# Performance work log

Measured on AMD Instinct MI355X. Metric: run time of the kernel, lower is better.

Reference implementation:

```python
import jax, jax.numpy as jnp
import numpy as np

B, T_ENC, T_DEC = 16, 256, 200
N_MELS, ENC_DIM, PRENET, ARNN, DRNN, ATT, NF, KS = 80, 512, 256, 1024, 1024, 128, 32, 31


def _init(k, shape, fan_in):
    return jax.random.normal(k, shape, dtype=jnp.float32) / np.sqrt(fan_in).astype(np.float32)


def setup_inputs() -> dict:
    ks = jax.random.split(jax.random.key(0), 20)
    return {
        "memory": jax.random.normal(ks[0], (B, T_ENC, ENC_DIM), jnp.float32),
        "decoder_inputs": jax.random.normal(ks[1], (B, N_MELS, T_DEC), jnp.float32),
        "memory_lengths": jax.random.randint(ks[2], (B,), T_ENC // 2, T_ENC + 1),
        "prenet_W1": _init(ks[3], (N_MELS, PRENET), N_MELS),
        "prenet_W2": _init(ks[4], (PRENET, PRENET), PRENET),
        "arnn_Wih": _init(ks[5], (PRENET + ENC_DIM, 4 * ARNN), PRENET + ENC_DIM),
        "arnn_Whh": _init(ks[6], (ARNN, 4 * ARNN), ARNN),
        "arnn_b": jnp.zeros((4 * ARNN,), jnp.float32),
        "Wq": _init(ks[7], (ARNN, ATT), ARNN),
        "Wmem": _init(ks[8], (ENC_DIM, ATT), ENC_DIM),
        "v_w": _init(ks[9], (ATT,), ATT),
        "loc_conv_W": _init(ks[10], (NF, 2, KS), 2 * KS),
        "loc_dense_W": _init(ks[11], (NF, ATT), NF),
        "drnn_Wih": _init(ks[12], (ARNN + ENC_DIM, 4 * DRNN), ARNN + ENC_DIM),
        "drnn_Whh": _init(ks[13], (DRNN, 4 * DRNN), DRNN),
        "drnn_b": jnp.zeros((4 * DRNN,), jnp.float32),
        "proj_W": _init(ks[14], (DRNN + ENC_DIM, N_MELS), DRNN + ENC_DIM),
        "proj_b": jnp.zeros((N_MELS,), jnp.float32),
        "gate_W": _init(ks[15], (DRNN + ENC_DIM, 1), DRNN + ENC_DIM),
        "gate_b": jnp.zeros((1,), jnp.float32),
    }


def _lstm_cell(x, h, c, Wih, Whh, b):
    z = x @ Wih + h @ Whh + b  # [B, 4H], torch gate order i,f,g,o
    i, f, g, o = jnp.split(z, 4, axis=-1)
    c_new = jax.nn.sigmoid(f) * c + jax.nn.sigmoid(i) * jnp.tanh(g)
    h_new = jax.nn.sigmoid(o) * jnp.tanh(c_new)
    return h_new, c_new


def reference(memory, decoder_inputs, memory_lengths, prenet_W1, prenet_W2,
              arnn_Wih, arnn_Whh, arnn_b, Wq, Wmem, v_w, loc_conv_W, loc_dense_W,
              drnn_Wih, drnn_Whh, drnn_b, proj_W, proj_b, gate_W, gate_b):
    dt = memory.dtype
    # parse_decoder_inputs + go-frame: [T_DEC+1, B, n_mels]
    di = jnp.transpose(decoder_inputs, (2, 0, 1))
    di = jnp.concatenate([jnp.zeros((1, B, N_MELS), dt), di], axis=0)
    # prenet (dropout hardcoded training=True in source; deterministic key here)
    k1, k2 = jax.random.split(jax.random.key(42))
    x = jax.nn.relu(di @ prenet_W1)
    x = x * jax.random.bernoulli(k1, 0.5, x.shape).astype(dt) * 2.0
    x = jax.nn.relu(x @ prenet_W2)
    x = x * jax.random.bernoulli(k2, 0.5, x.shape).astype(dt) * 2.0
    pre = x[:-1]  # [T_DEC, B, PRENET] (loop consumes first T_DEC frames)

    pm = memory @ Wmem  # processed_memory [B, T_enc, ATT]
    pad_mask = jnp.arange(T_ENC)[None, :] >= memory_lengths[:, None]  # [B, T_enc]
    pad = KS // 2

    def step(carry, xt):
        ah, ac, dh, dc, aw, awc, ctx = carry
        ah, ac = _lstm_cell(jnp.concatenate([xt, ctx], -1), ah, ac, arnn_Wih, arnn_Whh, arnn_b)
        # location-sensitive attention
        awcat = jnp.stack([aw, awc], axis=1)  # [B, 2, T_enc]
        loc = jax.lax.conv_general_dilated(awcat, loc_conv_W, (1,), [(pad, pad)],
                                           dimension_numbers=("NCH", "OIH", "NCH"))  # [B, NF, T_enc]
        loc = jnp.swapaxes(loc, 1, 2) @ loc_dense_W  # [B, T_enc, ATT]
        pq = ah @ Wq  # [B, ATT]
        e = jnp.tanh(pq[:, None, :] + loc + pm) @ v_w  # [B, T_enc]
        e = jnp.where(pad_mask, jnp.asarray(-1e9, dt), e)
        w = jax.nn.softmax(e, axis=1)
        ctx = jnp.einsum("bt,bte->be", w, memory)
        awc = awc + w
        dh, dc = _lstm_cell(jnp.concatenate([ah, ctx], -1), dh, dc, drnn_Wih, drnn_Whh, drnn_b)
        dhc = jnp.concatenate([dh, ctx], axis=1)
        mel = dhc @ proj_W + proj_b  # [B, n_mels]
        gate = (dhc @ gate_W + gate_b)[:, 0]  # [B]
        return (ah, ac, dh, dc, w, awc, ctx), (mel, gate, w)

    carry0 = (jnp.zeros((B, ARNN), dt), jnp.zeros((B, ARNN), dt),
              jnp.zeros((B, DRNN), dt), jnp.zeros((B, DRNN), dt),
              jnp.zeros((B, T_ENC), dt), jnp.zeros((B, T_ENC), dt),
              jnp.zeros((B, ENC_DIM), dt))
    _, (mels, gates, aligns) = jax.lax.scan(step, carry0, pre)
    mel_out = jnp.transpose(mels, (1, 2, 0))    # [B, n_mels, T_DEC]
    gate_out = jnp.transpose(gates, (1, 0))     # [B, T_DEC]
    align_out = jnp.transpose(aligns, (1, 0, 2))  # [B, T_DEC, T_enc]
    return mel_out, gate_out, align_out
```

## Files before the change

kernel.cpp:

```cpp
#include <hip/hip_runtime.h>
#include <stdint.h>

typedef unsigned short u16;
typedef _Float16 h2f16 __attribute__((ext_vector_type(2)));

#define BB    16
#define TENC  256
#define TDEC  200
#define NMELS 80
#define EDIM  512
#define PREN  256
#define ARN   1024
#define ATTN  128
#define NFILT 32
#define KSIZE 31

#define NBLK  256
#define NTHR  1024

#define OFF_AW     0
#define OFF_AWC    4096
#define OFF_AC     8192
#define OFF_DC     24576
#define OFF_XCAT1  49152
#define OFF_XCAT2  77824
#define STATE_F    118784
#define OFF_PRETU  118784
#define OFF_PMU    528384
#define OFF_Z      790528
#define OFF_PQP    1314816
#define OFF_EBUF   1347584
#define OFF_BAR    1351680

__host__ __device__ inline void tf2x32(uint32_t k0, uint32_t k1, uint32_t x0, uint32_t x1,
                                       uint32_t &y0, uint32_t &y1) {
  uint32_t ks2 = k0 ^ k1 ^ 0x1BD11BDAu;
  x0 += k0; x1 += k1;
  const int R0[4] = {13, 15, 26, 6};
  const int R1[4] = {17, 29, 16, 24};
#pragma unroll
  for (int g = 0; g < 5; ++g) {
    const int *R = (g & 1) ? R1 : R0;
#pragma unroll
    for (int i = 0; i < 4; ++i) {
      x0 += x1;
      x1 = (x1 << R[i]) | (x1 >> (32 - R[i]));
      x1 ^= x0;
    }
    switch (g) {
      case 0: x0 += k1;  x1 += ks2 + 1u; break;
      case 1: x0 += ks2; x1 += k0 + 2u;  break;
      case 2: x0 += k0;  x1 += k1 + 3u;  break;
      case 3: x0 += k1;  x1 += ks2 + 4u; break;
      case 4: x0 += ks2; x1 += k0 + 5u;  break;
    }
  }
  y0 = x0; y1 = x1;
}

__device__ inline bool keep_mask(uint32_t k0, uint32_t k1, uint32_t idx) {
  uint32_t y0, y1;
  tf2x32(k0, k1, 0u, idx, y0, y1);
  return (((y0 ^ y1) >> 31) == 0u);
}

__device__ inline float bf2f(u16 v) {
  union { uint32_t u; float f; } x;
  x.u = ((uint32_t)v) << 16;
  return x.f;
}
__device__ inline u16 f2bf(float f) {
  union { float f; uint32_t u; } x;
  x.f = f;
  uint32_t r = ((x.u >> 16) & 1u) + 0x7FFFu;
  return (u16)((x.u + r) >> 16);
}
__device__ inline float sigm(float x) { return 1.f / (1.f + __expf(-x)); }
__device__ inline float ftanh(float x) {
  x = fminf(fmaxf(x, -15.f), 15.f);
  float e = __expf(2.f * x);
  return (e - 1.f) / (e + 1.f);
}

__device__ inline uint32_t packh2(float a, float b) {
  h2f16 h; h[0] = (_Float16)a; h[1] = (_Float16)b;
  union { h2f16 h; uint32_t u; } x; x.h = h; return x.u;
}
__device__ inline h2f16 u2h2(uint32_t u) {
  union { uint32_t u; h2f16 h; } x; x.u = u; return x.h;
}
__device__ inline float fdot2(h2f16 a, h2f16 b, float c) {
#if __has_builtin(__builtin_amdgcn_fdot2)
  return __builtin_amdgcn_fdot2(a, b, c, false);
#else
  return (float)a[0] * (float)b[0] + (float)a[1] * (float)b[1] + c;
#endif
}

__device__ inline float cload(const float *p) {
  uint32_t u = __hip_atomic_load((uint32_t *)p, __ATOMIC_RELAXED,
                                 __HIP_MEMORY_SCOPE_SYSTEM);
  union { uint32_t u; float f; } x; x.u = u; return x.f;
}
__device__ inline void cstore(float *p, float v) {
  union { float f; uint32_t u; } x; x.f = v;
  __hip_atomic_store((uint32_t *)p, x.u, __ATOMIC_RELAXED,
                     __HIP_MEMORY_SCOPE_SYSTEM);
}

__device__ inline void gsync(unsigned int *bar, unsigned int e, int cb) {
  __syncthreads();
  if (threadIdx.x == 0) {
    asm volatile("s_waitcnt vmcnt(0)" ::: "memory");
    int g = cb & 7;
    unsigned int *arr = bar + g * 64;
    unsigned int *gct = bar + 512;
    unsigned int *rel = bar + 576 + g * 64;
    unsigned int old = __hip_atomic_fetch_add(arr, 1u, __ATOMIC_RELAXED,
                                              __HIP_MEMORY_SCOPE_SYSTEM);
    if (old == e * 32u - 1u) {
      unsigned int o2 = __hip_atomic_fetch_add(gct, 1u, __ATOMIC_RELAXED,
                                               __HIP_MEMORY_SCOPE_SYSTEM);
      if (o2 == e * 8u - 1u) {
#pragma unroll
        for (int g2 = 0; g2 < 8; ++g2)
          __hip_atomic_store(bar + 576 + g2 * 64, e, __ATOMIC_RELAXED,
                             __HIP_MEMORY_SCOPE_SYSTEM);
      }
    }
    while (__hip_atomic_load(rel, __ATOMIC_RELAXED, __HIP_MEMORY_SCOPE_SYSTEM) < e)
      __builtin_amdgcn_s_sleep(1);
  }
  __syncthreads();
}

__global__ __launch_bounds__(256) void k_prenet1(const float *__restrict__ dec_in,
                                                 const float *__restrict__ W1,
                                                 u16 *__restrict__ x1,
                                                 uint32_t k0, uint32_t k1) {
  int bid = blockIdx.x;
  int t = bid >> 4, b = bid & 15;
  int tid = threadIdx.x;
  __shared__ float di[NMELS];
  if (tid < NMELS)
    di[tid] = (t == 0) ? 0.f : dec_in[((size_t)b * NMELS + tid) * TDEC + (t - 1)];
  __syncthreads();
  int j = tid;
  float acc = 0.f;
#pragma unroll 4
  for (int m = 0; m < NMELS; ++m) acc += di[m] * W1[(size_t)m * PREN + j];
  acc = fmaxf(acc, 0.f);
  uint32_t idx = ((uint32_t)(t * BB + b)) * PREN + (uint32_t)j;
  acc = keep_mask(k0, k1, idx) ? acc * 2.f : 0.f;
  x1[(t * BB + b) * PREN + j] = f2bf(acc);
}

__global__ __launch_bounds__(256) void k_prenet2(const u16 *__restrict__ x1,
                                                 const float *__restrict__ W2,
                                                 u16 *__restrict__ preTu,
                                                 float *__restrict__ xpre0,
                                                 uint32_t k0, uint32_t k1) {
  int bid = blockIdx.x;
  int t = bid >> 4, b = bid & 15;
  int tid = threadIdx.x;
  __shared__ float xl[PREN];
  xl[tid] = bf2f(x1[(t * BB + b) * PREN + tid]);
  __syncthreads();
  int j = tid;
  float acc = 0.f;
#pragma unroll 4
  for (int k = 0; k < PREN; ++k) acc += xl[k] * W2[(size_t)k * PREN + j];
  acc = fmaxf(acc, 0.f);
  uint32_t idx = ((uint32_t)(t * BB + b)) * PREN + (uint32_t)j;
  acc = keep_mask(k0, k1, idx) ? acc * 2.f : 0.f;
  preTu[(size_t)t * 4096 + j * 16 + b] = f2bf(acc);
  if (t == 0) xpre0[j * 16 + b] = acc;
}

__global__ __launch_bounds__(256) void k_pm(const float *__restrict__ memory,
                                            const float *__restrict__ Wmem,
                                            u16 *__restrict__ pmu) {
  int p = blockIdx.x;
  int b = p & 15, jt = p >> 4;
  int tt = threadIdx.x;
  float acc[32];
#pragma unroll
  for (int j = 0; j < 32; ++j) acc[j] = 0.f;
  const float *mrow = memory + ((size_t)b * TENC + tt) * EDIM;
  const float *wb = Wmem + jt * 32;
  for (int e = 0; e < EDIM; ++e) {
    float mv = mrow[e];
    const float *wr = wb + (size_t)e * ATTN;
#pragma unroll
    for (int j = 0; j < 32; ++j) acc[j] += mv * wr[j];
  }
#pragma unroll
  for (int j = 0; j < 32; ++j)
    pmu[((size_t)(b * ATTN + jt * 32 + j)) * TENC + tt] = f2bf(acc[j]);
}

struct F2 { float x, y; };

union Scr {
  uint32_t xs1[112 * 16];
  uint32_t xs2[160 * 16];
  struct { F2 part[16 * 64]; float hn[64]; } al;
  struct {
    float aw_l[96], awc_l[96];
    float lc[64 * 33];
    float pq[128];
    float ep[64 * 17];
  } att;
  struct { float e_l[256]; float red[32]; float smax, sinv; float part[32 * 33]; } ctc;
  struct { float xl[1536]; float part[12 * 81]; } out;
};

struct KArgs {
  const float *memory; const int *mlen;
  const float *aWih, *aWhh, *ab;
  const float *Wq, *vw, *convW, *ldW;
  const float *dWih, *dWhh, *db;
  const float *projW, *projB, *gateW, *gateB;
  const u16 *preTu, *pmu;
  float *aw, *awc, *ac, *dc, *xcat1, *xcat2, *z, *pqp, *ebuf;
  unsigned int *bar;
  float *mel, *gate, *algn;
};

__global__ __launch_bounds__(NTHR) void k_persist(KArgs A) {
  __shared__ uint32_t w1h[112 * 128];
  __shared__ uint32_t w2h[160 * 128];
  __shared__ Scr s;
  const int cb = blockIdx.x;
  const int tid = threadIdx.x;
  const int q = cb >> 5;
  const int c = cb & 31;

  for (int i = tid; i < 112 * 128; i += NTHR) {
    int k2 = i >> 7, col = i & 127, cg = c * 128 + col;
    int r0 = q * 224 + k2 * 2;
    float f0 = (r0 < 768) ? A.aWih[(size_t)r0 * 4096 + cg]
                          : A.aWhh[(size_t)(r0 - 768) * 4096 + cg];
    float f1 = (r0 + 1 < 768) ? A.aWih[(size_t)(r0 + 1) * 4096 + cg]
                              : A.aWhh[(size_t)(r0 - 767) * 4096 + cg];
    w1h[i] = packh2(f0, f1);
  }
  for (int i = tid; i < 160 * 128; i += NTHR) {
    int k2 = i >> 7, col = i & 127, cg = c * 128 + col;
    int r0 = q * 320 + k2 * 2;
    float f0 = (r0 < 1536) ? A.dWih[(size_t)r0 * 4096 + cg]
                           : A.dWhh[(size_t)(r0 - 1536) * 4096 + cg];
    float f1 = (r0 + 1 < 1536) ? A.dWih[(size_t)(r0 + 1) * 4096 + cg]
                               : A.dWhh[(size_t)(r0 - 1535) * 4096 + cg];
    w2h[i] = packh2(f0, f1);
  }
  __syncthreads();

  unsigned int ep = 0;
  for (int t = 0; t < TDEC; ++t) {
    for (int i = tid; i < 112 * 16; i += NTHR) {
      int k2 = i >> 4, b = i & 15;
      const float *xr = A.xcat1 + (size_t)(q * 224 + k2 * 2) * 16 + b;
      s.xs1[i] = packh2(cload(xr), cload(xr + 16));
    }
    __syncthreads();
    {
      int col = tid & 127, bg = tid >> 7;
      float a0 = 0.f, a1 = 0.f;
      const uint32_t *wp = w1h + col;
      const uint32_t *xp = s.xs1 + bg * 2;
#pragma unroll 8
      for (int k2 = 0; k2 < 112; ++k2) {
        h2f16 w = u2h2(wp[k2 * 128]);
        a0 = fdot2(w, u2h2(xp[k2 * 16]), a0);
        a1 = fdot2(w, u2h2(xp[k2 * 16 + 1]), a1);
      }
      int cg = c * 128 + col;
      cstore(&A.z[((size_t)q * 16 + bg * 2    ) * 4096 + cg], a0);
      cstore(&A.z[((size_t)q * 16 + bg * 2 + 1) * 4096 + cg], a1);
    }
    gsync(A.bar, ++ep, cb);

    {
      int b = cb & 15, ug = cb >> 4;
      {
        int u_l = tid & 63, j = tid >> 6;
        int kc = j & 7, gh = j >> 3;
        const float *zb = A.z + ((size_t)(kc * 16 + b)) * 4096 + gh * 2048 + (ug * 64 + u_l);
        F2 p; p.x = cload(zb); p.y = cload(zb + 1024);
        s.al.part[j * 64 + u_l] = p;
      }
      __syncthreads();
      if (tid < 64) {
        int uu = ug * 64 + tid;
        float g0 = 0.f, g1 = 0.f, g2 = 0.f, g3 = 0.f;
#pragma unroll
        for (int kc = 0; kc < 8; ++kc) {
          F2 v0 = s.al.part[kc * 64 + tid];
          F2 v1 = s.al.part[(8 + kc) * 64 + tid];
          g0 += v0.x; g1 += v0.y; g2 += v1.x; g3 += v1.y;
        }
        float zi = g0 + A.ab[uu], zf = g1 + A.ab[1024 + uu];
        float zg = g2 + A.ab[2048 + uu], zo = g3 + A.ab[3072 + uu];
        float cn = sigm(zf) * A.ac[b * 1024 + uu] + sigm(zi) * ftanh(zg);
        float hn = sigm(zo) * ftanh(cn);
        A.ac[b * 1024 + uu] = cn;
        cstore(&A.xcat1[(size_t)(768 + uu) * 16 + b], hn);
        cstore(&A.xcat2[(size_t)uu * 16 + b], hn);
        s.al.hn[tid] = hn;
      }
      __syncthreads();
      if (tid < 128) {
        float a = 0.f;
        const float *wq = A.Wq + (size_t)(ug * 64) * 128 + tid;
#pragma unroll 4
        for (int k = 0; k < 64; ++k) a += s.al.hn[k] * wq[(size_t)k * 128];
        cstore(&A.pqp[(size_t)(b * 16 + ug) * 128 + tid], a);
      }
    }
    gsync(A.bar, ++ep, cb);

    if (cb < 64) {
      int b = cb & 15, tq = cb >> 4;
      if (tid < 96) {
        int gi = tq * 64 - 16 + tid;
        bool ok = (gi >= 0 && gi < 256);
        s.att.aw_l[tid]  = ok ? cload(&A.aw[b * 256 + gi])  : 0.f;
        s.att.awc_l[tid] = ok ? cload(&A.awc[b * 256 + gi]) : 0.f;
      }
      if (tid >= 128 && tid < 256) {
        int j = tid - 128;
        float sum = 0.f;
#pragma unroll
        for (int g = 0; g < 16; ++g) sum += cload(&A.pqp[(size_t)(b * 16 + g) * 128 + j]);
        s.att.pq[j] = sum;
      }
      __syncthreads();
      {
        int tt_l = tid & 63, fg = tid >> 6;
        int f0 = fg * 2;
        float a0 = 0.f, a1 = 0.f;
        for (int k = 0; k < KSIZE; ++k) {
          float av = s.att.aw_l[tt_l + k + 1];
          float cv = s.att.awc_l[tt_l + k + 1];
          a0 += av * A.convW[f0 * 62 + k]       + cv * A.convW[f0 * 62 + 31 + k];
          a1 += av * A.convW[(f0 + 1) * 62 + k] + cv * A.convW[(f0 + 1) * 62 + 31 + k];
        }
        s.att.lc[tt_l * 33 + f0]     = a0;
        s.att.lc[tt_l * 33 + f0 + 1] = a1;
      }
      __syncthreads();
      {
        int tt_l = tid & 63, g = tid >> 6;
        int tt = tq * 64 + tt_l, j0 = g * 8;
        float acc[8] = {0, 0, 0, 0, 0, 0, 0, 0};
        for (int f = 0; f < NFILT; ++f) {
          float lv = s.att.lc[tt_l * 33 + f];
          const float *lw = A.ldW + f * ATTN + j0;
#pragma unroll
          for (int jj = 0; jj < 8; ++jj) acc[jj] += lv * lw[jj];
        }
        float es = 0.f;
#pragma unroll
        for (int jj = 0; jj < 8; ++jj) {
          float sv = acc[jj] + s.att.pq[j0 + jj]
                   + bf2f(A.pmu[((size_t)(b * 128 + j0 + jj)) * 256 + tt]);
          es += ftanh(sv) * A.vw[j0 + jj];
        }
        s.att.ep[tt_l * 17 + g] = es;
      }
      __syncthreads();
      if (tid < 64) {
        float e = 0.f;
#pragma unroll
        for (int g = 0; g < 16; ++g) e += s.att.ep[tid * 17 + g];
        int tt = tq * 64 + tid;
        if (tt >= A.mlen[b]) e = -1e9f;
        cstore(&A.ebuf[b * 256 + tt], e);
      }
    }
    gsync(A.bar, ++ep, cb);

    {
      int b = cb & 15, ec = cb >> 4;
      if (tid < 256) s.ctc.e_l[tid] = cload(&A.ebuf[b * 256 + tid]);
      __syncthreads();
      if (tid < 32) {
        float m = -1e30f;
#pragma unroll
        for (int i = 0; i < 8; ++i) m = fmaxf(m, s.ctc.e_l[tid * 8 + i]);
        s.ctc.red[tid] = m;
      }
      __syncthreads();
      if (tid == 0) {
        float m = -1e30f;
        for (int i = 0; i < 32; ++i) m = fmaxf(m, s.ctc.red[i]);
        s.ctc.smax = m;
      }
      __syncthreads();
      if (tid < 256) s.ctc.e_l[tid] = __expf(s.ctc.e_l[tid] - s.ctc.smax);
      __syncthreads();
      if (tid < 32) {
        float sm = 0.f;
#pragma unroll
        for (int i = 0; i < 8; ++i) sm += s.ctc.e_l[tid * 8 + i];
        s.ctc.red[tid] = sm;
      }
      __syncthreads();
      if (tid == 0) {
        float sm = 0.f;
        for (int i = 0; i < 32; ++i) sm += s.ctc.red[i];
        s.ctc.sinv = 1.f / sm;
      }
      __syncthreads();
      if (tid < 256) s.ctc.e_l[tid] *= s.ctc.sinv;
      __syncthreads();
      if (ec == 0 && tid < 256) {
        float w = s.ctc.e_l[tid];
        cstore(&A.aw[b * 256 + tid], w);
        cstore(&A.awc[b * 256 + tid], cload(&A.awc[b * 256 + tid]) + w);
        A.algn[((size_t)b * TDEC + t) * TENC + tid] = w;
      }
      {
        int e_l = tid & 31, sub = tid >> 5;
        const float *mp = A.memory + ((size_t)(b * 256) + sub * 8) * 512 + ec * 32 + e_l;
        float a = 0.f;
#pragma unroll
        for (int i = 0; i < 8; ++i) a += s.ctc.e_l[sub * 8 + i] * mp[(size_t)i * 512];
        s.ctc.part[e_l * 33 + sub] = a;
      }
      __syncthreads();
      if (tid < 32) {
        float sum = 0.f;
#pragma unroll
        for (int i = 0; i < 32; ++i) sum += s.ctc.part[tid * 33 + i];
        int eg = ec * 32 + tid;
        cstore(&A.xcat1[(size_t)(256 + eg) * 16 + b], sum);
        cstore(&A.xcat2[(size_t)(1024 + eg) * 16 + b], sum);
      }
    }
    gsync(A.bar, ++ep, cb);

    for (int i = tid; i < 160 * 16; i += NTHR) {
      int k2 = i >> 4, b = i & 15;
      const float *xr = A.xcat2 + (size_t)(q * 320 + k2 * 2) * 16 + b;
      s.xs2[i] = packh2(cload(xr), cload(xr + 16));
    }
    __syncthreads();
    {
      int col = tid & 127, bg = tid >> 7;
      float a0 = 0.f, a1 = 0.f;
      const uint32_t *wp = w2h + col;
      const uint32_t *xp = s.xs2 + bg * 2;
#pragma unroll 8
      for (int k2 = 0; k2 < 160; ++k2) {
        h2f16 w = u2h2(wp[k2 * 128]);
        a0 = fdot2(w, u2h2(xp[k2 * 16]), a0);
        a1 = fdot2(w, u2h2(xp[k2 * 16 + 1]), a1);
      }
      int cg = c * 128 + col;
      cstore(&A.z[((size_t)q * 16 + bg * 2    ) * 4096 + cg], a0);
      cstore(&A.z[((size_t)q * 16 + bg * 2 + 1) * 4096 + cg], a1);
    }
    gsync(A.bar, ++ep, cb);

    if (cb < 16) {
      int b = cb;
      {
        int u = tid;
        float zi = 0.f, zf = 0.f, zg = 0.f, zo = 0.f;
        for (int kc = 0; kc < 8; ++kc) {
          const float *zb = A.z + ((size_t)(kc * 16 + b)) * 4096;
          zi += cload(zb + u); zf += cload(zb + u + 1024);
          zg += cload(zb + u + 2048); zo += cload(zb + u + 3072);
        }
        zi += A.db[u]; zf += A.db[u + 1024]; zg += A.db[u + 2048]; zo += A.db[u + 3072];
        float cn = sigm(zf) * A.dc[b * 1024 + u] + sigm(zi) * ftanh(zg);
        float hn = sigm(zo) * ftanh(cn);
        A.dc[b * 1024 + u] = cn;
        cstore(&A.xcat2[(size_t)(1536 + u) * 16 + b], hn);
        s.out.xl[u] = hn;
      }
      if (tid < 512) s.out.xl[1024 + tid] = cload(&A.xcat2[(size_t)(1024 + tid) * 16 + b]);
      __syncthreads();
      if (tid < 960) {
        int col = tid % 80, kc = tid / 80;
        const float *wp = A.projW + (size_t)(kc * 128) * 80 + col;
        const float *xk = s.out.xl + kc * 128;
        float a = 0.f;
#pragma unroll 4
        for (int kk = 0; kk < 128; ++kk) a += xk[kk] * wp[(size_t)kk * 80];
        s.out.part[kc * 81 + col] = a;
      } else if (tid < 972) {
        int kc = tid - 960;
        const float *xk = s.out.xl + kc * 128;
        const float *gk = A.gateW + kc * 128;
        float a = 0.f;
#pragma unroll 4
        for (int kk = 0; kk < 128; ++kk) a += xk[kk] * gk[kk];
        s.out.part[kc * 81 + 80] = a;
      }
      __syncthreads();
      if (tid < 81) {
        float sum = 0.f;
#pragma unroll
        for (int kc = 0; kc < 12; ++kc) sum += s.out.part[kc * 81 + tid];
        if (tid < 80) A.mel[((size_t)b * 80 + tid) * TDEC + t] = sum + A.projB[tid];
        else          A.gate[(size_t)b * TDEC + t] = sum + A.gateB[0];
      }
    } else if (cb < 20) {
      if (t + 1 < TDEC) {
        int idx = (cb - 16) * 1024 + tid;
        cstore(&A.xcat1[idx], bf2f(A.preTu[(size_t)(t + 1) * 4096 + idx]));
      }
    }
    gsync(A.bar, ++ep, cb);
  }
}

extern "C" void kernel_launch(void *const *d_in, const int *in_sizes, int n_in,
                              void *d_out, int out_size, void *d_ws, size_t ws_size,
                              hipStream_t stream) {
  (void)in_sizes; (void)n_in; (void)out_size; (void)ws_size;
  const float *memory = (const float *)d_in[0];
  const float *dec_in = (const float *)d_in[1];
  const int   *mlen   = (const int *)d_in[2];
  const float *pw1    = (const float *)d_in[3];
  const float *pw2    = (const float *)d_in[4];
  const float *aWih   = (const float *)d_in[5];
  const float *aWhh   = (const float *)d_in[6];
  const float *ab     = (const float *)d_in[7];
  const float *wq     = (const float *)d_in[8];
  const float *wmem   = (const float *)d_in[9];
  const float *vw     = (const float *)d_in[10];
  const float *convW  = (const float *)d_in[11];
  const float *ldW    = (const float *)d_in[12];
  const float *dWih   = (const float *)d_in[13];
  const float *dWhh   = (const float *)d_in[14];
  const float *db     = (const float *)d_in[15];
  const float *projW  = (const float *)d_in[16];
  const float *projB  = (const float *)d_in[17];
  const float *gateW  = (const float *)d_in[18];
  const float *gateB  = (const float *)d_in[19];

  float *out_mel  = (float *)d_out;
  float *out_gate = out_mel + (size_t)16 * 80 * 200;
  float *out_algn = out_gate + (size_t)16 * 200;

  float *ws = (float *)d_ws;
  float *aw    = ws + OFF_AW;
  float *awc   = ws + OFF_AWC;
  float *ac    = ws + OFF_AC;
  float *dc    = ws + OFF_DC;
  float *xcat1 = ws + OFF_XCAT1;
  float *xcat2 = ws + OFF_XCAT2;
  float *xpre  = xcat1;
  u16 *preTu = (u16 *)(ws + OFF_PRETU);
  u16 *pmu   = (u16 *)(ws + OFF_PMU);
  float *z    = ws + OFF_Z;
  float *pqp  = ws + OFF_PQP;
  float *ebuf = ws + OFF_EBUF;
  unsigned int *bar = (unsigned int *)(ws + OFF_BAR);
  u16 *x1u   = (u16 *)z;

  hipMemsetAsync(ws, 0, STATE_F * sizeof(float), stream);
  hipMemsetAsync(bar, 0, 2048 * sizeof(unsigned int), stream);

  uint32_t K1a, K1b, K2a, K2b;
  tf2x32(0u, 42u, 0u, 0u, K1a, K1b);
  tf2x32(0u, 42u, 0u, 1u, K2a, K2b);

  k_prenet1<<<TDEC * BB, 256, 0, stream>>>(dec_in, pw1, x1u, K1a, K1b);
  k_prenet2<<<TDEC * BB, 256, 0, stream>>>(x1u, pw2, preTu, xpre, K2a, K2b);
  k_pm<<<64, 256, 0, stream>>>(memory, wmem, pmu);

  KArgs ka;
  ka.memory = memory; ka.mlen = mlen;
  ka.aWih = aWih; ka.aWhh = aWhh; ka.ab = ab;
  ka.Wq = wq; ka.vw = vw; ka.convW = convW; ka.ldW = ldW;
  ka.dWih = dWih; ka.dWhh = dWhh; ka.db = db;
  ka.projW = projW; ka.projB = projB; ka.gateW = gateW; ka.gateB = gateB;
  ka.preTu = preTu; ka.pmu = pmu;
  ka.aw = aw; ka.awc = awc; ka.ac = ac; ka.dc = dc;
  ka.xcat1 = xcat1; ka.xcat2 = xcat2; ka.z = z; ka.pqp = pqp; ka.ebuf = ebuf;
  ka.bar = bar;
  ka.mel = out_mel; ka.gate = out_gate; ka.algn = out_algn;

  void *kp[] = { &ka };
  hipLaunchCooperativeKernel((void *)k_persist, dim3(NBLK), dim3(NTHR), kp, 0, stream);
}
```

Baseline: 27.28 ms.

## Restructure persistent decoder to unit-sliced LSTM columns with fewer grid barriers

```diff
diff --git a/kernel.cpp b/kernel.cpp
--- a/kernel.cpp
+++ b/kernel.cpp
@@ -18,19 +18,16 @@
 #define NBLK  256
 #define NTHR  1024
 
-#define OFF_AW     0
-#define OFF_AWC    4096
-#define OFF_AC     8192
-#define OFF_DC     24576
-#define OFF_XCAT1  49152
-#define OFF_XCAT2  77824
-#define STATE_F    118784
-#define OFF_PRETU  118784
-#define OFF_PMU    528384
-#define OFF_Z      790528
-#define OFF_PQP    1314816
-#define OFF_EBUF   1347584
-#define OFF_BAR    1351680
+#define OFF_X1H   0
+#define OFF_X2H   22528
+#define OFF_AHF   51200
+#define OFF_CTXF  67584
+#define OFF_DHF   83968
+#define OFF_BAR   100352
+#define STATE_F   102400
+#define OFF_PRETU 102400
+#define OFF_PMU   512000
+#define OFF_X1U   774144
 
 __host__ __device__ inline void tf2x32(uint32_t k0, uint32_t k1, uint32_t x0, uint32_t x1,
                                        uint32_t &y0, uint32_t &y1) {
@@ -98,14 +95,20 @@
 }
 
 __device__ inline float cload(const float *p) {
-  uint32_t u = __hip_atomic_load((uint32_t *)p, __ATOMIC_RELAXED,
-                                 __HIP_MEMORY_SCOPE_SYSTEM);
+  uint32_t u = __hip_atomic_load((const uint32_t *)p, __ATOMIC_RELAXED,
+                                 __HIP_MEMORY_SCOPE_AGENT);
   union { uint32_t u; float f; } x; x.u = u; return x.f;
 }
 __device__ inline void cstore(float *p, float v) {
   union { float f; uint32_t u; } x; x.f = v;
   __hip_atomic_store((uint32_t *)p, x.u, __ATOMIC_RELAXED,
-                     __HIP_MEMORY_SCOPE_SYSTEM);
+                     __HIP_MEMORY_SCOPE_AGENT);
+}
+__device__ inline uint32_t cload_u32(const uint32_t *p) {
+  return __hip_atomic_load(p, __ATOMIC_RELAXED, __HIP_MEMORY_SCOPE_AGENT);
+}
+__device__ inline void cstore_u32(uint32_t *p, uint32_t v) {
+  __hip_atomic_store(p, v, __ATOMIC_RELAXED, __HIP_MEMORY_SCOPE_AGENT);
 }
 
 __device__ inline void gsync(unsigned int *bar, unsigned int e, int cb) {
@@ -117,18 +120,18 @@
     unsigned int *gct = bar + 512;
     unsigned int *rel = bar + 576 + g * 64;
     unsigned int old = __hip_atomic_fetch_add(arr, 1u, __ATOMIC_RELAXED,
-                                              __HIP_MEMORY_SCOPE_SYSTEM);
+                                              __HIP_MEMORY_SCOPE_AGENT);
     if (old == e * 32u - 1u) {
       unsigned int o2 = __hip_atomic_fetch_add(gct, 1u, __ATOMIC_RELAXED,
-                                               __HIP_MEMORY_SCOPE_SYSTEM);
+                                               __HIP_MEMORY_SCOPE_AGENT);
       if (o2 == e * 8u - 1u) {
 #pragma unroll
         for (int g2 = 0; g2 < 8; ++g2)
           __hip_atomic_store(bar + 576 + g2 * 64, e, __ATOMIC_RELAXED,
-                             __HIP_MEMORY_SCOPE_SYSTEM);
+                             __HIP_MEMORY_SCOPE_AGENT);
       }
     }
-    while (__hip_atomic_load(rel, __ATOMIC_RELAXED, __HIP_MEMORY_SCOPE_SYSTEM) < e)
+    while (__hip_atomic_load(rel, __ATOMIC_RELAXED, __HIP_MEMORY_SCOPE_AGENT) < e)
       __builtin_amdgcn_s_sleep(1);
   }
   __syncthreads();
@@ -157,8 +160,8 @@
 
 __global__ __launch_bounds__(256) void k_prenet2(const u16 *__restrict__ x1,
                                                  const float *__restrict__ W2,
-                                                 u16 *__restrict__ preTu,
-                                                 float *__restrict__ xpre0,
+                                                 uint32_t *__restrict__ preTuP,
+                                                 uint32_t *__restrict__ x1hPre,
                                                  uint32_t k0, uint32_t k1) {
   int bid = blockIdx.x;
   int t = bid >> 4, b = bid & 15;
@@ -173,8 +176,12 @@
   acc = fmaxf(acc, 0.f);
   uint32_t idx = ((uint32_t)(t * BB + b)) * PREN + (uint32_t)j;
   acc = keep_mask(k0, k1, idx) ? acc * 2.f : 0.f;
-  preTu[(size_t)t * 4096 + j * 16 + b] = f2bf(acc);
-  if (t == 0) xpre0[j * 16 + b] = acc;
+  float accN = __shfl_down(acc, 1);
+  if (!(j & 1)) {
+    uint32_t pk = packh2(acc, accN);
+    preTuP[(size_t)t * 2048 + (j >> 1) * 16 + b] = pk;
+    if (t == 0) x1hPre[(j >> 1) * 16 + b] = pk;
+  }
 }
 
 __global__ __launch_bounds__(256) void k_pm(const float *__restrict__ memory,
@@ -199,19 +206,16 @@
     pmu[((size_t)(b * ATTN + jt * 32 + j)) * TENC + tt] = f2bf(acc[j]);
 }
 
-struct F2 { float x, y; };
-
 union Scr {
-  uint32_t xs1[112 * 16];
-  uint32_t xs2[160 * 16];
-  struct { F2 part[16 * 64]; float hn[64]; } al;
+  struct { uint32_t xs[2][1088]; float zr[1024]; } z;
   struct {
-    float aw_l[96], awc_l[96];
-    float lc[64 * 33];
+    float ah[1024];
+    union { float pqp[1024]; float cp[2][512]; } u;
     float pq[128];
-    float ep[64 * 17];
-  } att;
-  struct { float e_l[256]; float red[32]; float smax, sinv; float part[32 * 33]; } ctc;
+    float e_l[256];
+    float red[32];
+    float smax, sinv;
+  } at;
   struct { float xl[1536]; float part[12 * 81]; } out;
 };
 
@@ -221,301 +225,318 @@
   const float *Wq, *vw, *convW, *ldW;
   const float *dWih, *dWhh, *db;
   const float *projW, *projB, *gateW, *gateB;
-  const u16 *preTu, *pmu;
-  float *aw, *awc, *ac, *dc, *xcat1, *xcat2, *z, *pqp, *ebuf;
+  const uint32_t *preTuP; const u16 *pmu;
+  uint32_t *x1h, *x2h;
+  float *ahf, *ctxf, *dhf;
   unsigned int *bar;
   float *mel, *gate, *algn;
 };
 
+__device__ inline void do_out(const KArgs &A, Scr &s, int b, int tm, int tid) {
+  s.out.xl[tid] = cload(A.dhf + (size_t)tid * 16 + b);
+  if (tid < 512) s.out.xl[1024 + tid] = cload(A.ctxf + (size_t)(tm & 1) * 8192 + tid * 16 + b);
+  __syncthreads();
+  if (tid < 960) {
+    int col = tid % 80, kc = tid / 80;
+    const float *wp = A.projW + (size_t)(kc * 128) * 80 + col;
+    const float *xk = s.out.xl + kc * 128;
+    float a = 0.f;
+#pragma unroll 4
+    for (int kk = 0; kk < 128; ++kk) a += xk[kk] * wp[(size_t)kk * 80];
+    s.out.part[kc * 81 + col] = a;
+  } else if (tid < 972) {
+    int kc = tid - 960;
+    const float *xk = s.out.xl + kc * 128;
+    const float *gk = A.gateW + kc * 128;
+    float a = 0.f;
+#pragma unroll 4
+    for (int kk = 0; kk < 128; ++kk) a += xk[kk] * gk[kk];
+    s.out.part[kc * 81 + 80] = a;
+  }
+  __syncthreads();
+  if (tid < 81) {
+    float sum = 0.f;
+#pragma unroll
+    for (int kc = 0; kc < 12; ++kc) sum += s.out.part[kc * 81 + tid];
+    if (tid < 80) A.mel[((size_t)b * 80 + tid) * TDEC + tm] = sum + A.projB[tid];
+    else          A.gate[(size_t)b * TDEC + tm] = sum + A.gateB[0];
+  }
+}
+
 __global__ __launch_bounds__(NTHR) void k_persist(KArgs A) {
-  __shared__ uint32_t w1h[112 * 128];
-  __shared__ uint32_t w2h[160 * 128];
+  __shared__ uint32_t w1h[16 * 900];
+  __shared__ uint32_t w2h[16 * 1284];
+  __shared__ float awA[288], awC[288];
   __shared__ Scr s;
   const int cb = blockIdx.x;
   const int tid = threadIdx.x;
-  const int q = cb >> 5;
-  const int c = cb & 31;
-
-  for (int i = tid; i < 112 * 128; i += NTHR) {
-    int k2 = i >> 7, col = i & 127, cg = c * 128 + col;
-    int r0 = q * 224 + k2 * 2;
-    float f0 = (r0 < 768) ? A.aWih[(size_t)r0 * 4096 + cg]
-                          : A.aWhh[(size_t)(r0 - 768) * 4096 + cg];
-    float f1 = (r0 + 1 < 768) ? A.aWih[(size_t)(r0 + 1) * 4096 + cg]
-                              : A.aWhh[(size_t)(r0 - 767) * 4096 + cg];
-    w1h[i] = packh2(f0, f1);
-  }
-  for (int i = tid; i < 160 * 128; i += NTHR) {
-    int k2 = i >> 7, col = i & 127, cg = c * 128 + col;
-    int r0 = q * 320 + k2 * 2;
-    float f0 = (r0 < 1536) ? A.dWih[(size_t)r0 * 4096 + cg]
-                           : A.dWhh[(size_t)(r0 - 1536) * 4096 + cg];
-    float f1 = (r0 + 1 < 1536) ? A.dWih[(size_t)(r0 + 1) * 4096 + cg]
-                               : A.dWhh[(size_t)(r0 - 1535) * 4096 + cg];
-    w2h[i] = packh2(f0, f1);
-  }
+
+  for (int i = tid; i < 16 * 896; i += NTHR) {
+    int k2 = i >> 4, cl = i & 15;
+    int gcol = cb * 4 + (cl & 3) + (cl >> 2) * 1024;
+    int r0 = k2 * 2;
+    float f0 = (r0 < 768) ? A.aWih[(size_t)r0 * 4096 + gcol]
+                          : A.aWhh[(size_t)(r0 - 768) * 4096 + gcol];
+    float f1 = (r0 + 1 < 768) ? A.aWih[(size_t)(r0 + 1) * 4096 + gcol]
+                              : A.aWhh[(size_t)(r0 - 767) * 4096 + gcol];
+    w1h[cl * 900 + k2] = packh2(f0, f1);
+  }
+  for (int i = tid; i < 16 * 1280; i += NTHR) {
+    int k2 = i >> 4, cl = i & 15;
+    int gcol = cb * 4 + (cl & 3) + (cl >> 2) * 1024;
+    int r0 = k2 * 2;
+    float f0 = (r0 < 1536) ? A.dWih[(size_t)r0 * 4096 + gcol]
+                           : A.dWhh[(size_t)(r0 - 1536) * 4096 + gcol];
+    float f1 = (r0 + 1 < 1536) ? A.dWih[(size_t)(r0 + 1) * 4096 + gcol]
+                               : A.dWhh[(size_t)(r0 - 1535) * 4096 + gcol];
+    w2h[cl * 1284 + k2] = packh2(f0, f1);
+  }
+  if (tid < 288) { awA[tid] = 0.f; awC[tid] = 0.f; }
   __syncthreads();
 
+  const int cl = tid & 15, bq = (tid >> 4) & 15, sl = tid >> 8;
+  const int k2s = tid >> 4, bs = tid & 15;
+  float acR = 0.f, dcR = 0.f;
   unsigned int ep = 0;
+
   for (int t = 0; t < TDEC; ++t) {
-    for (int i = tid; i < 112 * 16; i += NTHR) {
-      int k2 = i >> 4, b = i & 15;
-      const float *xr = A.xcat1 + (size_t)(q * 224 + k2 * 2) * 16 + b;
-      s.xs1[i] = packh2(cload(xr), cload(xr + 16));
-    }
-    __syncthreads();
+    const int p = t & 1, rp = p ^ 1;
+
     {
-      int col = tid & 127, bg = tid >> 7;
-      float a0 = 0.f, a1 = 0.f;
-      const uint32_t *wp = w1h + col;
-      const uint32_t *xp = s.xs1 + bg * 2;
-#pragma unroll 8
-      for (int k2 = 0; k2 < 112; ++k2) {
-        h2f16 w = u2h2(wp[k2 * 128]);
-        a0 = fdot2(w, u2h2(xp[k2 * 16]), a0);
-        a1 = fdot2(w, u2h2(xp[k2 * 16 + 1]), a1);
-      }
-      int cg = c * 128 + col;
-      cstore(&A.z[((size_t)q * 16 + bg * 2    ) * 4096 + cg], a0);
-      cstore(&A.z[((size_t)q * 16 + bg * 2 + 1) * 4096 + cg], a1);
+      uint32_t v[14];
+#pragma unroll
+      for (int c = 0; c < 14; ++c) {
+        int K2 = c * 64 + k2s;
+        int pp = K2 < 384 ? K2 : 384 + rp * 512 + (K2 - 384);
+        v[c] = cload_u32(A.x1h + (size_t)pp * 16 + bs);
+      }
+      float acc = 0.f;
+      const uint32_t *wcol = w1h + cl * 900;
+#pragma unroll
+      for (int c = 0; c < 14; ++c) {
+        s.z.xs[c & 1][bs * 68 + k2s] = v[c];
+        __syncthreads();
+        const uint32_t *xr = s.z.xs[c & 1] + bq * 68 + sl * 16;
+        const uint32_t *wr = wcol + c * 64 + sl * 16;
+#pragma unroll
+        for (int kk = 0; kk < 16; kk += 4) {
+          uint4 wv = *(const uint4 *)(wr + kk);
+          uint4 xv = *(const uint4 *)(xr + kk);
+          acc = fdot2(u2h2(wv.x), u2h2(xv.x), acc);
+          acc = fdot2(u2h2(wv.y), u2h2(xv.y), acc);
+          acc = fdot2(u2h2(wv.z), u2h2(xv.z), acc);
+          acc = fdot2(u2h2(wv.w), u2h2(xv.w), acc);
+        }
+      }
+      s.z.zr[sl * 256 + cl * 16 + bq] = acc;
+      __syncthreads();
+      if (tid < 64) {
+        int ul = tid >> 4, bb = tid & 15, u = cb * 4 + ul;
+        float zg4[4];
+#pragma unroll
+        for (int gate = 0; gate < 4; ++gate) {
+          int cc = gate * 4 + ul;
+          float zs = A.ab[(size_t)gate * 1024 + u];
+#pragma unroll
+          for (int slc = 0; slc < 4; ++slc) zs += s.z.zr[slc * 256 + cc * 16 + bb];
+          zg4[gate] = zs;
+        }
+        float cn = sigm(zg4[1]) * acR + sigm(zg4[0]) * ftanh(zg4[2]);
+        float hn = sigm(zg4[3]) * ftanh(cn);
+        acR = cn;
+        cstore(A.ahf + (size_t)u * 16 + bb, hn);
+        float hn2 = __shfl_down(hn, 16);
+        if (!(ul & 1)) {
+          uint32_t pk = packh2(hn, hn2);
+          cstore_u32(A.x1h + (size_t)(384 + p * 512 + (u >> 1)) * 16 + bb, pk);
+          cstore_u32(A.x2h + (size_t)(u >> 1) * 16 + bb, pk);
+        }
+      }
     }
     gsync(A.bar, ++ep, cb);
 
-    {
-      int b = cb & 15, ug = cb >> 4;
+    if (cb < 16) {
+      int b = cb;
+      int len = A.mlen[b];
+      s.at.ah[tid] = cload(A.ahf + (size_t)tid * 16 + b);
+      __syncthreads();
       {
-        int u_l = tid & 63, j = tid >> 6;
-        int kc = j & 7, gh = j >> 3;
-        const float *zb = A.z + ((size_t)(kc * 16 + b)) * 4096 + gh * 2048 + (ug * 64 + u_l);
-        F2 p; p.x = cload(zb); p.y = cload(zb + 1024);
-        s.al.part[j * 64 + u_l] = p;
-      }
-      __syncthreads();
-      if (tid < 64) {
-        int uu = ug * 64 + tid;
-        float g0 = 0.f, g1 = 0.f, g2 = 0.f, g3 = 0.f;
-#pragma unroll
-        for (int kc = 0; kc < 8; ++kc) {
-          F2 v0 = s.al.part[kc * 64 + tid];
-          F2 v1 = s.al.part[(8 + kc) * 64 + tid];
-          g0 += v0.x; g1 += v0.y; g2 += v1.x; g3 += v1.y;
-        }
-        float zi = g0 + A.ab[uu], zf = g1 + A.ab[1024 + uu];
-        float zg = g2 + A.ab[2048 + uu], zo = g3 + A.ab[3072 + uu];
-        float cn = sigm(zf) * A.ac[b * 1024 + uu] + sigm(zi) * ftanh(zg);
-        float hn = sigm(zo) * ftanh(cn);
-        A.ac[b * 1024 + uu] = cn;
-        cstore(&A.xcat1[(size_t)(768 + uu) * 16 + b], hn);
-        cstore(&A.xcat2[(size_t)uu * 16 + b], hn);
-        s.al.hn[tid] = hn;
+        int j = tid & 127, kc = tid >> 7;
+        float a = 0.f;
+        const float *wq = A.Wq + (size_t)(kc * 128) * ATTN + j;
+#pragma unroll 4
+        for (int k = 0; k < 128; ++k) a += s.at.ah[kc * 128 + k] * wq[(size_t)k * ATTN];
+        s.at.u.pqp[j * 8 + kc] = a;
       }
       __syncthreads();
       if (tid < 128) {
+        float sm = 0.f;
+#pragma unroll
+        for (int kc = 0; kc < 8; ++kc) sm += s.at.u.pqp[tid * 8 + kc];
+        s.at.pq[tid] = sm;
+      }
+      __syncthreads();
+      int tt = tid >> 2, g = tid & 3;
+      float lc[8];
+#pragma unroll
+      for (int f8 = 0; f8 < 8; ++f8) lc[f8] = 0.f;
+      for (int k = 0; k < KSIZE; ++k) {
+        float av = awA[tt + k + 1], cv = awC[tt + k + 1];
+#pragma unroll
+        for (int f8 = 0; f8 < 8; ++f8) {
+          int f = g * 8 + f8;
+          lc[f8] += av * A.convW[f * 62 + k] + cv * A.convW[f * 62 + 31 + k];
+        }
+      }
+      float es = 0.f;
+#pragma unroll
+      for (int half = 0; half < 2; ++half) {
+        float loc[16];
+#pragma unroll
+        for (int jj = 0; jj < 16; ++jj) loc[jj] = 0.f;
+#pragma unroll
+        for (int r = 0; r < 4; ++r) {
+          int fg = g ^ r;
+#pragma unroll
+          for (int f8 = 0; f8 < 8; ++f8) {
+            float lv = __shfl_xor(lc[f8], r);
+            const float4 *lw4 =
+                (const float4 *)(A.ldW + (size_t)(fg * 8 + f8) * ATTN + g * 32 + half * 16);
+            float4 w0 = lw4[0], w1v = lw4[1], w2v = lw4[2], w3v = lw4[3];
+            loc[0] += lv * w0.x;  loc[1] += lv * w0.y;  loc[2] += lv * w0.z;  loc[3] += lv * w0.w;
+            loc[4] += lv * w1v.x; loc[5] += lv * w1v.y; loc[6] += lv * w1v.z; loc[7] += lv * w1v.w;
+            loc[8] += lv * w2v.x; loc[9] += lv * w2v.y; loc[10]+= lv * w2v.z; loc[11]+= lv * w2v.w;
+            loc[12]+= lv * w3v.x; loc[13]+= lv * w3v.y; loc[14]+= lv * w3v.z; loc[15]+= lv * w3v.w;
+          }
+        }
+#pragma unroll
+        for (int jj = 0; jj < 16; ++jj) {
+          int j = g * 32 + half * 16 + jj;
+          float sv = loc[jj] + s.at.pq[j] + bf2f(A.pmu[((size_t)(b * 128 + j)) * 256 + tt]);
+          es += ftanh(sv) * A.vw[j];
+        }
+      }
+      es += __shfl_xor(es, 1);
+      es += __shfl_xor(es, 2);
+      if (g == 0) s.at.e_l[tt] = (tt >= len) ? -1e9f : es;
+      __syncthreads();
+      if (tid < 32) {
+        float m = -1e30f;
+#pragma unroll
+        for (int i = 0; i < 8; ++i) m = fmaxf(m, s.at.e_l[tid * 8 + i]);
+        s.at.red[tid] = m;
+      }
+      __syncthreads();
+      if (tid == 0) {
+        float m = -1e30f;
+        for (int i = 0; i < 32; ++i) m = fmaxf(m, s.at.red[i]);
+        s.at.smax = m;
+      }
+      __syncthreads();
+      if (tid < 256) s.at.e_l[tid] = __expf(s.at.e_l[tid] - s.at.smax);
+      __syncthreads();
+      if (tid < 32) {
+        float sm = 0.f;
+#pragma unroll
+        for (int i = 0; i < 8; ++i) sm += s.at.e_l[tid * 8 + i];
+        s.at.red[tid] = sm;
+      }
+      __syncthreads();
+      if (tid == 0) {
+        float sm = 0.f;
+        for (int i = 0; i < 32; ++i) sm += s.at.red[i];
+        s.at.sinv = 1.f / sm;
+      }
+      __syncthreads();
+      if (tid < 256) {
+        float w = s.at.e_l[tid] * s.at.sinv;
+        s.at.e_l[tid] = w;
+        awA[16 + tid] = w;
+        awC[16 + tid] += w;
+        A.algn[((size_t)b * TDEC + t) * TENC + tid] = w;
+      }
+      __syncthreads();
+      {
+        int e = tid & 511, h = tid >> 9;
+        int t0 = h * 128, t1 = min(len, (h + 1) * 128);
         float a = 0.f;
-        const float *wq = A.Wq + (size_t)(ug * 64) * 128 + tid;
-#pragma unroll 4
-        for (int k = 0; k < 64; ++k) a += s.al.hn[k] * wq[(size_t)k * 128];
-        cstore(&A.pqp[(size_t)(b * 16 + ug) * 128 + tid], a);
+        for (int ti = t0; ti < t1; ++ti)
+          a += s.at.e_l[ti] * A.memory[((size_t)b * TENC + ti) * EDIM + e];
+        s.at.u.cp[h][e] = a;
+      }
+      __syncthreads();
+      if (tid < 512) {
+        float v = s.at.u.cp[0][tid] + s.at.u.cp[1][tid];
+        cstore(A.ctxf + (size_t)p * 8192 + tid * 16 + b, v);
+        float v2 = __shfl_down(v, 1);
+        if (!(tid & 1)) {
+          uint32_t pk = packh2(v, v2);
+          cstore_u32(A.x1h + (size_t)(128 + (tid >> 1)) * 16 + b, pk);
+          cstore_u32(A.x2h + (size_t)(512 + (tid >> 1)) * 16 + b, pk);
+        }
+      }
+    } else if (cb < 32) {
+      if (t > 0) do_out(A, s, cb - 16, t - 1, tid);
+    } else if (cb < 34) {
+      if (t + 1 < TDEC) {
+        int i = (cb - 32) * 1024 + tid;
+        cstore_u32(A.x1h + i, cload_u32(A.preTuP + (size_t)(t + 1) * 2048 + i));
       }
     }
     gsync(A.bar, ++ep, cb);
 
-    if (cb < 64) {
-      int b = cb & 15, tq = cb >> 4;
-      if (tid < 96) {
-        int gi = tq * 64 - 16 + tid;
-        bool ok = (gi >= 0 && gi < 256);
-        s.att.aw_l[tid]  = ok ? cload(&A.aw[b * 256 + gi])  : 0.f;
-        s.att.awc_l[tid] = ok ? cload(&A.awc[b * 256 + gi]) : 0.f;
-      }
-      if (tid >= 128 && tid < 256) {
-        int j = tid - 128;
-        float sum = 0.f;
-#pragma unroll
-        for (int g = 0; g < 16; ++g) sum += cload(&A.pqp[(size_t)(b * 16 + g) * 128 + j]);
-        s.att.pq[j] = sum;
-      }
-      __syncthreads();
-      {
-        int tt_l = tid & 63, fg = tid >> 6;
-        int f0 = fg * 2;
-        float a0 = 0.f, a1 = 0.f;
-        for (int k = 0; k < KSIZE; ++k) {
-          float av = s.att.aw_l[tt_l + k + 1];
-          float cv = s.att.awc_l[tt_l + k + 1];
-          a0 += av * A.convW[f0 * 62 + k]       + cv * A.convW[f0 * 62 + 31 + k];
-          a1 += av * A.convW[(f0 + 1) * 62 + k] + cv * A.convW[(f0 + 1) * 62 + 31 + k];
-        }
-        s.att.lc[tt_l * 33 + f0]     = a0;
-        s.att.lc[tt_l * 33 + f0 + 1] = a1;
-      }
-      __syncthreads();
-      {
-        int tt_l = tid & 63, g = tid >> 6;
-        int tt = tq * 64 + tt_l, j0 = g * 8;
-        float acc[8] = {0, 0, 0, 0, 0, 0, 0, 0};
-        for (int f = 0; f < NFILT; ++f) {
-          float lv = s.att.lc[tt_l * 33 + f];
-          const float *lw = A.ldW + f * ATTN + j0;
-#pragma unroll
-          for (int jj = 0; jj < 8; ++jj) acc[jj] += lv * lw[jj];
-        }
-        float es = 0.f;
-#pragma unroll
-        for (int jj = 0; jj < 8; ++jj) {
-          float sv = acc[jj] + s.att.pq[j0 + jj]
-                   + bf2f(A.pmu[((size_t)(b * 128 + j0 + jj)) * 256 + tt]);
-          es += ftanh(sv) * A.vw[j0 + jj];
-        }
-        s.att.ep[tt_l * 17 + g] = es;
-      }
+    {
+      uint32_t v2[20];
+#pragma unroll
+      for (int c = 0; c < 20; ++c) {
+        int K2 = c * 64 + k2s;
+        int pp = K2 < 768 ? K2 : 768 + rp * 512 + (K2 - 768);
+        v2[c] = cload_u32(A.x2h + (size_t)pp * 16 + bs);
+      }
+      float acc = 0.f;
+      const uint32_t *wcol = w2h + cl * 1284;
+#pragma unroll
+      for (int c = 0; c < 20; ++c) {
+        s.z.xs[c & 1][bs * 68 + k2s] = v2[c];
+        __syncthreads();
+        const uint32_t *xr = s.z.xs[c & 1] + bq * 68 + sl * 16;
+        const uint32_t *wr = wcol + c * 64 + sl * 16;
+#pragma unroll
+        for (int kk = 0; kk < 16; kk += 4) {
+          uint4 wv = *(const uint4 *)(wr + kk);
+          uint4 xv = *(const uint4 *)(xr + kk);
+          acc = fdot2(u2h2(wv.x), u2h2(xv.x), acc);
+          acc = fdot2(u2h2(wv.y), u2h2(xv.y), acc);
+          acc = fdot2(u2h2(wv.z), u2h2(xv.z), acc);
+          acc = fdot2(u2h2(wv.w), u2h2(xv.w), acc);
+        }
+      }
+      s.z.zr[sl * 256 + cl * 16 + bq] = acc;
       __syncthreads();
       if (tid < 64) {
-        float e = 0.f;
-#pragma unroll
-        for (int g = 0; g < 16; ++g) e += s.att.ep[tid * 17 + g];
-        int tt = tq * 64 + tid;
-        if (tt >= A.mlen[b]) e = -1e9f;
-        cstore(&A.ebuf[b * 256 + tt], e);
+        int ul = tid >> 4, bb = tid & 15, u = cb * 4 + ul;
+        float zg4[4];
+#pragma unroll
+        for (int gate = 0; gate < 4; ++gate) {
+          int cc = gate * 4 + ul;
+          float zs = A.db[(size_t)gate * 1024 + u];
+#pragma unroll
+          for (int slc = 0; slc < 4; ++slc) zs += s.z.zr[slc * 256 + cc * 16 + bb];
+          zg4[gate] = zs;
+        }
+        float cn = sigm(zg4[1]) * dcR + sigm(zg4[0]) * ftanh(zg4[2]);
+        float hn = sigm(zg4[3]) * ftanh(cn);
+        dcR = cn;
+        cstore(A.dhf + (size_t)u * 16 + bb, hn);
+        float hn2 = __shfl_down(hn, 16);
+        if (!(ul & 1))
+          cstore_u32(A.x2h + (size_t)(768 + p * 512 + (u >> 1)) * 16 + bb, packh2(hn, hn2));
       }
     }
     gsync(A.bar, ++ep, cb);
-
-    {
-      int b = cb & 15, ec = cb >> 4;
-      if (tid < 256) s.ctc.e_l[tid] = cload(&A.ebuf[b * 256 + tid]);
-      __syncthreads();
-      if (tid < 32) {
-        float m = -1e30f;
-#pragma unroll
-        for (int i = 0; i < 8; ++i) m = fmaxf(m, s.ctc.e_l[tid * 8 + i]);
-        s.ctc.red[tid] = m;
-      }
-      __syncthreads();
-      if (tid == 0) {
-        float m = -1e30f;
-        for (int i = 0; i < 32; ++i) m = fmaxf(m, s.ctc.red[i]);
-        s.ctc.smax = m;
-      }
-      __syncthreads();
-      if (tid < 256) s.ctc.e_l[tid] = __expf(s.ctc.e_l[tid] - s.ctc.smax);
-      __syncthreads();
-      if (tid < 32) {
-        float sm = 0.f;
-#pragma unroll
-        for (int i = 0; i < 8; ++i) sm += s.ctc.e_l[tid * 8 + i];
-        s.ctc.red[tid] = sm;
-      }
-      __syncthreads();
-      if (tid == 0) {
-        float sm = 0.f;
-        for (int i = 0; i < 32; ++i) sm += s.ctc.red[i];
-        s.ctc.sinv = 1.f / sm;
-      }
-      __syncthreads();
-      if (tid < 256) s.ctc.e_l[tid] *= s.ctc.sinv;
-      __syncthreads();
-      if (ec == 0 && tid < 256) {
-        float w = s.ctc.e_l[tid];
-        cstore(&A.aw[b * 256 + tid], w);
-        cstore(&A.awc[b * 256 + tid], cload(&A.awc[b * 256 + tid]) + w);
-        A.algn[((size_t)b * TDEC + t) * TENC + tid] = w;
-      }
-      {
-        int e_l = tid & 31, sub = tid >> 5;
-        const float *mp = A.memory + ((size_t)(b * 256) + sub * 8) * 512 + ec * 32 + e_l;
-        float a = 0.f;
-#pragma unroll
-        for (int i = 0; i < 8; ++i) a += s.ctc.e_l[sub * 8 + i] * mp[(size_t)i * 512];
-        s.ctc.part[e_l * 33 + sub] = a;
-      }
-      __syncthreads();
-      if (tid < 32) {
-        float sum = 0.f;
-#pragma unroll
-        for (int i = 0; i < 32; ++i) sum += s.ctc.part[tid * 33 + i];
-        int eg = ec * 32 + tid;
-        cstore(&A.xcat1[(size_t)(256 + eg) * 16 + b], sum);
-        cstore(&A.xcat2[(size_t)(1024 + eg) * 16 + b], sum);
-      }
-    }
-    gsync(A.bar, ++ep, cb);
-
-    for (int i = tid; i < 160 * 16; i += NTHR) {
-      int k2 = i >> 4, b = i & 15;
-      const float *xr = A.xcat2 + (size_t)(q * 320 + k2 * 2) * 16 + b;
-      s.xs2[i] = packh2(cload(xr), cload(xr + 16));
-    }
-    __syncthreads();
-    {
-      int col = tid & 127, bg = tid >> 7;
-      float a0 = 0.f, a1 = 0.f;
-      const uint32_t *wp = w2h + col;
-      const uint32_t *xp = s.xs2 + bg * 2;
-#pragma unroll 8
-      for (int k2 = 0; k2 < 160; ++k2) {
-        h2f16 w = u2h2(wp[k2 * 128]);
-        a0 = fdot2(w, u2h2(xp[k2 * 16]), a0);
-        a1 = fdot2(w, u2h2(xp[k2 * 16 + 1]), a1);
-      }
-      int cg = c * 128 + col;
-      cstore(&A.z[((size_t)q * 16 + bg * 2    ) * 4096 + cg], a0);
-      cstore(&A.z[((size_t)q * 16 + bg * 2 + 1) * 4096 + cg], a1);
-    }
-    gsync(A.bar, ++ep, cb);
-
-    if (cb < 16) {
-      int b = cb;
-      {
-        int u = tid;
-        float zi = 0.f, zf = 0.f, zg = 0.f, zo = 0.f;
-        for (int kc = 0; kc < 8; ++kc) {
-          const float *zb = A.z + ((size_t)(kc * 16 + b)) * 4096;
-          zi += cload(zb + u); zf += cload(zb + u + 1024);
-          zg += cload(zb + u + 2048); zo += cload(zb + u + 3072);
-        }
-        zi += A.db[u]; zf += A.db[u + 1024]; zg += A.db[u + 2048]; zo += A.db[u + 3072];
-        float cn = sigm(zf) * A.dc[b * 1024 + u] + sigm(zi) * ftanh(zg);
-        float hn = sigm(zo) * ftanh(cn);
-        A.dc[b * 1024 + u] = cn;
-        cstore(&A.xcat2[(size_t)(1536 + u) * 16 + b], hn);
-        s.out.xl[u] = hn;
-      }
-      if (tid < 512) s.out.xl[1024 + tid] = cload(&A.xcat2[(size_t)(1024 + tid) * 16 + b]);
-      __syncthreads();
-      if (tid < 960) {
-        int col = tid % 80, kc = tid / 80;
-        const float *wp = A.projW + (size_t)(kc * 128) * 80 + col;
-        const float *xk = s.out.xl + kc * 128;
-        float a = 0.f;
-#pragma unroll 4
-        for (int kk = 0; kk < 128; ++kk) a += xk[kk] * wp[(size_t)kk * 80];
-        s.out.part[kc * 81 + col] = a;
-      } else if (tid < 972) {
-        int kc = tid - 960;
-        const float *xk = s.out.xl + kc * 128;
-        const float *gk = A.gateW + kc * 128;
-        float a = 0.f;
-#pragma unroll 4
-        for (int kk = 0; kk < 128; ++kk) a += xk[kk] * gk[kk];
-        s.out.part[kc * 81 + 80] = a;
-      }
-      __syncthreads();
-      if (tid < 81) {
-        float sum = 0.f;
-#pragma unroll
-        for (int kc = 0; kc < 12; ++kc) sum += s.out.part[kc * 81 + tid];
-        if (tid < 80) A.mel[((size_t)b * 80 + tid) * TDEC + t] = sum + A.projB[tid];
-        else          A.gate[(size_t)b * TDEC + t] = sum + A.gateB[0];
-      }
-    } else if (cb < 20) {
-      if (t + 1 < TDEC) {
-        int idx = (cb - 16) * 1024 + tid;
-        cstore(&A.xcat1[idx], bf2f(A.preTu[(size_t)(t + 1) * 4096 + idx]));
-      }
-    }
-    gsync(A.bar, ++ep, cb);
-  }
+  }
+
+  if (cb >= 16 && cb < 32) do_out(A, s, cb - 16, TDEC - 1, tid);
 }
 
 extern "C" void kernel_launch(void *const *d_in, const int *in_sizes, int n_in,
@@ -548,20 +569,15 @@
   float *out_algn = out_gate + (size_t)16 * 200;
 
   float *ws = (float *)d_ws;
-  float *aw    = ws + OFF_AW;
-  float *awc   = ws + OFF_AWC;
-  float *ac    = ws + OFF_AC;
-  float *dc    = ws + OFF_DC;
-  float *xcat1 = ws + OFF_XCAT1;
-  float *xcat2 = ws + OFF_XCAT2;
-  float *xpre  = xcat1;
-  u16 *preTu = (u16 *)(ws + OFF_PRETU);
-  u16 *pmu   = (u16 *)(ws + OFF_PMU);
-  float *z    = ws + OFF_Z;
-  float *pqp  = ws + OFF_PQP;
-  float *ebuf = ws + OFF_EBUF;
+  uint32_t *x1h    = (uint32_t *)(ws + OFF_X1H);
+  uint32_t *x2h    = (uint32_t *)(ws + OFF_X2H);
+  float    *ahf    = ws + OFF_AHF;
+  float    *ctxf   = ws + OFF_CTXF;
+  float    *dhf    = ws + OFF_DHF;
   unsigned int *bar = (unsigned int *)(ws + OFF_BAR);
-  u16 *x1u   = (u16 *)z;
+  uint32_t *preTuP = (uint32_t *)(ws + OFF_PRETU);
+  u16      *pmu    = (u16 *)(ws + OFF_PMU);
+  u16      *x1u    = (u16 *)(ws + OFF_X1U);
 
   hipMemsetAsync(ws, 0, STATE_F * sizeof(float), stream);
   hipMemsetAsync(bar, 0, 2048 * sizeof(unsigned int), stream);
@@ -571,7 +587,7 @@
   tf2x32(0u, 42u, 0u, 1u, K2a, K2b);
 
   k_prenet1<<<TDEC * BB, 256, 0, stream>>>(dec_in, pw1, x1u, K1a, K1b);
-  k_prenet2<<<TDEC * BB, 256, 0, stream>>>(x1u, pw2, preTu, xpre, K2a, K2b);
+  k_prenet2<<<TDEC * BB, 256, 0, stream>>>(x1u, pw2, preTuP, x1h, K2a, K2b);
   k_pm<<<64, 256, 0, stream>>>(memory, wmem, pmu);
 
   KArgs ka;
@@ -580,9 +596,9 @@
   ka.Wq = wq; ka.vw = vw; ka.convW = convW; ka.ldW = ldW;
   ka.dWih = dWih; ka.dWhh = dWhh; ka.db = db;
   ka.projW = projW; ka.projB = projB; ka.gateW = gateW; ka.gateB = gateB;
-  ka.preTu = preTu; ka.pmu = pmu;
-  ka.aw = aw; ka.awc = awc; ka.ac = ac; ka.dc = dc;
-  ka.xcat1 = xcat1; ka.xcat2 = xcat2; ka.z = z; ka.pqp = pqp; ka.ebuf = ebuf;
+  ka.preTuP = preTuP; ka.pmu = pmu;
+  ka.x1h = x1h; ka.x2h = x2h;
+  ka.ahf = ahf; ka.ctxf = ctxf; ka.dhf = dhf;
   ka.bar = bar;
   ka.mel = out_mel; ka.gate = out_gate; ka.algn = out_algn;
 
```

Result: slower. 57.75 ms (+111.7%).
